# Kernel optimization log

Hardware: AMD Instinct MI355X
Metric: run time of the kernel (lower is better)

The kernel has to match this reference:

```python
import jax, jax.numpy as jnp
import numpy as np

B = 1024      # batch
L = 50        # max_seq_len
D = 128       # embed_dim
NV = 8        # n_v vertical filters
NH = 16       # n_h horizontal filters per height
NU = 100000   # num_users
NI = 500000   # num_items


def setup_inputs() -> dict:
    key = jax.random.key(0)
    ks = jax.random.split(key, 8)
    user_ids = jax.random.randint(ks[0], (B,), 0, NU)
    item_seq = jax.random.randint(ks[1], (B, L), 0, NI)
    user_emb = jax.random.normal(ks[2], (NU, D), jnp.float32) * 0.02
    item_emb = jax.random.normal(ks[3], (NI, D), jnp.float32) * 0.02
    item_emb = item_emb.at[0].set(0.0)  # padding_idx=0 -> zero row
    # vertical Conv2d(1, NV, (L, 1)) weight, flattened over the (L,1) kernel
    Wv = jax.random.normal(ks[4], (NV, L), jnp.float32) * 0.05
    bv = jnp.zeros((NV,), jnp.float32)
    # horizontal filters: height h = i+1 kernel (h, D); stored zero-padded to length L
    hmask = (jnp.arange(L)[None, :] < (jnp.arange(L)[:, None] + 1)).astype(jnp.float32)  # [L_heights, L_taps]
    Wh = jax.random.normal(ks[5], (L, NH, L, D), jnp.float32) * 0.05
    Wh = Wh * hmask[:, None, :, None]
    bh = jnp.zeros((L, NH), jnp.float32)
    fc_W = jax.random.normal(ks[6], (NV * D + NH * L, D), jnp.float32) * 0.02
    fc_b = jnp.zeros((D,), jnp.float32)
    return dict(user_ids=user_ids, item_seq=item_seq, user_emb=user_emb,
                item_emb=item_emb, Wv=Wv, bv=bv, Wh=Wh, bh=bh,
                fc_W=fc_W, fc_b=fc_b)


def reference(user_ids, item_seq, user_emb, item_emb, Wv, bv, Wh, bh, fc_W, fc_b):
    P_u = user_emb[user_ids]                      # [B, D]
    E = item_emb[item_seq]                        # [B, L, D]
    # vertical conv: kernel (L,1) -> per-output-channel weighted sum over time
    o_v = (jnp.einsum('btd,vt->bvd', E, Wv) + bv[None, :, None]).reshape(B, NV * D)
    # horizontal convs for all heights in one batched conv over zero-padded kernels
    Epad = jnp.pad(E, ((0, 0), (0, L - 1), (0, 0)))       # [B, 2L-1, D]
    x = Epad[:, None, :, :]                               # NCHW: [B,1,2L-1,D]
    k = Wh.reshape(L * NH, 1, L, D)                       # OIHW
    conv = jax.lax.conv_general_dilated(
        x, k, window_strides=(1, 1), padding='VALID',
        dimension_numbers=('NCHW', 'OIHW', 'NCHW'))       # [B, L*NH, L, 1]
    conv = conv[..., 0].reshape(B, L, NH, L) + bh[None, :, :, None]
    h = jax.nn.relu(conv)
    # height h=i+1 is only valid at positions t <= L-1-i (valid conv length L-h+1)
    valid = jnp.arange(L)[None, :] <= (L - 1 - jnp.arange(L))[:, None]  # [heights, t]
    h = jnp.where(valid[None, :, None, :], h, -jnp.inf)
    o_h = h.max(axis=-1).reshape(B, L * NH)               # max-pool over valid time
    o = jnp.concatenate([o_v, o_h], axis=1)               # dropout in eval mode = identity
    z = jax.nn.relu(o @ fc_W + fc_b)
    return jnp.concatenate([z, P_u], axis=1)              # [B, 2D]
```

## Files before the change

kernel.cpp:

```cpp
#include <hip/hip_runtime.h>
#include <stdint.h>

typedef float  f32x4  __attribute__((ext_vector_type(4)));
typedef short  bf16x8 __attribute__((ext_vector_type(8)));

#define NCOL 800
#define NPAD 896
#define KDIM 6400
#define KFC  1856

__device__ __forceinline__ unsigned short f2bf(float f) {
  unsigned int u = __float_as_uint(f);
  return (unsigned short)((u + 0x7FFFu + ((u >> 16) & 1u)) >> 16);
}
__device__ __forceinline__ float bf2f(unsigned short s) {
  return __uint_as_float(((unsigned int)s) << 16);
}
__device__ __forceinline__ void gload16(const void* g, void* lds) {
  __builtin_amdgcn_global_load_lds(
      (const __attribute__((address_space(1))) unsigned int*)g,
      (__attribute__((address_space(3))) unsigned int*)lds, 16, 0, 0);
}
__device__ __forceinline__ void barrier_fenced() {
  __builtin_amdgcn_sched_barrier(0);
  asm volatile("s_barrier" ::: "memory");
  __builtin_amdgcn_sched_barrier(0);
}

__global__ void k_prep(const int* __restrict__ iseq, const float* __restrict__ iemb,
                       unsigned short* __restrict__ Ebf,
                       const float* __restrict__ Wh, unsigned short* __restrict__ Wbf,
                       const float* __restrict__ fcW, unsigned short* __restrict__ Bt,
                       unsigned int* __restrict__ o_h, float* __restrict__ facc) {
  __shared__ float tile[32][33];
  const int blk = blockIdx.x;
  if (blk < 1024) {
    int b = blk;
    for (int idx = threadIdx.x; idx < 1600; idx += 256) {
      int tt = idx >> 5, dq = idx & 31;
      int row = iseq[b * 50 + tt];
      float4 v = *reinterpret_cast<const float4*>(iemb + (size_t)row * 128 + dq * 4);
      unsigned int lo = (unsigned int)f2bf(v.x) | ((unsigned int)f2bf(v.y) << 16);
      unsigned int hi = (unsigned int)f2bf(v.z) | ((unsigned int)f2bf(v.w) << 16);
      *reinterpret_cast<uint2*>(Ebf + (size_t)b * KDIM + tt * 128 + dq * 4) = make_uint2(lo, hi);
    }
  } else if (blk < 1024 + NPAD) {
    int n = blk - 1024;
    unsigned short* dst = Wbf + (size_t)n * KDIM;
    if (n >= NCOL) {
      uint4 z = make_uint4(0, 0, 0, 0);
      for (int idx = threadIdx.x; idx < KDIM / 8; idx += 256)
        reinterpret_cast<uint4*>(dst)[idx] = z;
    } else {
      const float* src = Wh + (size_t)n * KDIM;
      for (int idx = threadIdx.x; idx < KDIM / 4; idx += 256) {
        float4 v = reinterpret_cast<const float4*>(src)[idx];
        unsigned int lo = (unsigned int)f2bf(v.x) | ((unsigned int)f2bf(v.y) << 16);
        unsigned int hi = (unsigned int)f2bf(v.z) | ((unsigned int)f2bf(v.w) << 16);
        reinterpret_cast<uint2*>(dst)[idx] = make_uint2(lo, hi);
      }
    }
  } else if (blk < 1024 + NPAD + 232) {
    int idx = blk - 1024 - NPAD;
    int k0 = (idx % 58) * 32, d0 = (idx / 58) * 32;
    int tx = threadIdx.x & 31, ty = threadIdx.x >> 5;
#pragma unroll
    for (int it = 0; it < 4; it++) {
      int k = k0 + ty + it * 8;
      tile[ty + it * 8][tx] = (k < 1824) ? fcW[(size_t)k * 128 + d0 + tx] : 0.f;
    }
    __syncthreads();
#pragma unroll
    for (int it = 0; it < 4; it++) {
      int d = d0 + ty + it * 8;
      Bt[(size_t)d * KFC + k0 + tx] = f2bf(tile[tx][ty + it * 8]);
    }
  } else if (blk < 1024 + NPAD + 232 + 400) {
    int base = (blk - 1024 - NPAD - 232) * 2048;
    uint2 z2 = make_uint2(0, 0);
    reinterpret_cast<uint2*>(o_h + base)[threadIdx.x] = z2;
    reinterpret_cast<uint2*>(o_h + base + 512)[threadIdx.x] = z2;
    reinterpret_cast<uint2*>(o_h + base + 1024)[threadIdx.x] = z2;
    reinterpret_cast<uint2*>(o_h + base + 1536)[threadIdx.x] = z2;
  } else {
    int base = (blk - 1024 - NPAD - 232 - 400) * 2048;
    float2 z2 = make_float2(0.f, 0.f);
    reinterpret_cast<float2*>(facc + base)[threadIdx.x] = z2;
    reinterpret_cast<float2*>(facc + base + 512)[threadIdx.x] = z2;
    reinterpret_cast<float2*>(facc + base + 1024)[threadIdx.x] = z2;
    reinterpret_cast<float2*>(facc + base + 1536)[threadIdx.x] = z2;
  }
}

__launch_bounds__(256, 2)
__global__ void k_conv(const unsigned short* __restrict__ Ebf,
                       const unsigned short* __restrict__ Wbf,
                       const float* __restrict__ bh,
                       unsigned int* __restrict__ o_h) {
  __shared__ alignas(16) unsigned short As[2][128 * 64];
  __shared__ alignas(16) unsigned short Bs[2][128 * 64];

  const int tid = threadIdx.x;
  const int wid = tid >> 6, lane = tid & 63;
  const int r = lane & 15, kg = lane >> 4;
  const int wm = wid >> 1, wn = wid & 1;
  const int mt = blockIdx.x, nt = blockIdx.y, s = blockIdx.z;

  const int lmax = min(nt * 8 + 7, 49);
  const int shi = 49 - nt * 8;
  if (s > shi) return;

  const int Rloc = lane >> 3;
  const int cph = lane & 7;

  const f32x4 z4 = {0.f, 0.f, 0.f, 0.f};
  f32x4 acc[4][4];
#pragma unroll
  for (int m = 0; m < 4; m++)
#pragma unroll
    for (int n = 0; n < 4; n++) acc[m][n] = z4;

  auto STAGE = [&](int buf, int kk) {
    const int Rb = wid * 32;
#pragma unroll
    for (int ia = 0; ia < 4; ia++) {
      int R = Rb + ia * 8 + Rloc;
      const unsigned short* src = Ebf + (size_t)(mt * 128 + R) * KDIM + s * 128 + kk * 64
                                      + ((cph ^ (R & 7)) * 8);
      gload16(src, &As[buf][(Rb + ia * 8) * 64]);
    }
#pragma unroll
    for (int ia = 0; ia < 4; ia++) {
      int R = Rb + ia * 8 + Rloc;
      const unsigned short* src = Wbf + (size_t)(nt * 128 + R) * KDIM + kk * 64
                                      + ((cph ^ (R & 7)) * 8);
      gload16(src, &Bs[buf][(Rb + ia * 8) * 64]);
    }
  };

  auto COMPUTE = [&](int buf) {
#pragma unroll
    for (int ks = 0; ks < 2; ks++) {
      bf16x8 af[4], bfr[4];
      const int sw = ((ks * 4 + kg) ^ (r & 7)) * 8;
#pragma unroll
      for (int m = 0; m < 4; m++)
        af[m] = *reinterpret_cast<const bf16x8*>(&As[buf][(wm * 64 + m * 16 + r) * 64 + sw]);
#pragma unroll
      for (int n = 0; n < 4; n++)
        bfr[n] = *reinterpret_cast<const bf16x8*>(&Bs[buf][(wn * 64 + n * 16 + r) * 64 + sw]);
#pragma unroll
      for (int m = 0; m < 4; m++)
#pragma unroll
        for (int n = 0; n < 4; n++)
          acc[m][n] = __builtin_amdgcn_mfma_f32_16x16x32_bf16(af[m], bfr[n], acc[m][n], 0, 0, 0);
    }
  };

  const int nk = min(50 - s, lmax + 1) * 2;
  STAGE(0, 0);
  int cur = 0;
  for (int kk = 0; kk < nk; kk++) {
    const bool has_next = (kk + 1 < nk);
    if (has_next) {
      STAGE(cur ^ 1, kk + 1);
      asm volatile("s_waitcnt vmcnt(8)" ::: "memory");
    } else {
      asm volatile("s_waitcnt vmcnt(0)" ::: "memory");
    }
    barrier_fenced();
    __builtin_amdgcn_s_setprio(1);
    COMPUTE(cur);
    __builtin_amdgcn_s_setprio(0);
    barrier_fenced();
    cur ^= 1;
  }

#pragma unroll
  for (int n = 0; n < 4; n++) {
    int ng = nt * 128 + wn * 64 + n * 16 + r;
    if (ng < NCOL && s <= 49 - (ng >> 4)) {
      float bhv = bh[ng];
#pragma unroll
      for (int m = 0; m < 4; m++) {
        int b = mt * 128 + wm * 64 + m * 16 + kg * 4;
#pragma unroll
        for (int q = 0; q < 4; q++) {
          float v = fmaxf(acc[m][n][q] + bhv, 0.f);
          atomicMax(&o_h[(size_t)(b + q) * NCOL + ng], __float_as_uint(v));
        }
      }
    }
  }
}

__global__ void k_ovcvt(const unsigned short* __restrict__ Ebf,
                        const float* __restrict__ Wv, const float* __restrict__ bv,
                        const unsigned int* __restrict__ o_h,
                        unsigned short* __restrict__ o_bf) {
  int b = blockIdx.x;
  const unsigned short* e = Ebf + (size_t)b * KDIM;
  for (int rep = 0; rep < 2; rep++) {
    int idx2 = rep * 256 + threadIdx.x;
    int v = idx2 >> 6;
    int dp = (idx2 & 63) * 2;
    float a0 = bv[v], a1 = a0;
    for (int tt = 0; tt < 50; tt++) {
      float w = Wv[v * 50 + tt];
      a0 += bf2f(e[tt * 128 + dp]) * w;
      a1 += bf2f(e[tt * 128 + dp + 1]) * w;
    }
    unsigned int pk = (unsigned int)f2bf(a0) | ((unsigned int)f2bf(a1) << 16);
    reinterpret_cast<unsigned int*>(o_bf + (size_t)b * KFC)[idx2] = pk;
  }
  const unsigned int* src = o_h + (size_t)b * NCOL;
  unsigned int* dst = reinterpret_cast<unsigned int*>(o_bf + (size_t)b * KFC + 1024);
  for (int i = threadIdx.x; i < 416; i += 256) {
    int j0 = 2 * i, j1 = j0 + 1;
    unsigned int lo = (j0 < NCOL) ? f2bf(__uint_as_float(src[j0])) : 0;
    unsigned int hi = (j1 < NCOL) ? f2bf(__uint_as_float(src[j1])) : 0;
    dst[i] = lo | (hi << 16);
  }
}

__launch_bounds__(256, 2)
__global__ void k_fc2(const unsigned short* __restrict__ o_bf,
                      const unsigned short* __restrict__ Bt,
                      float* __restrict__ facc) {
  __shared__ alignas(16) unsigned short As[2][128 * 64];
  __shared__ alignas(16) unsigned short Bs[2][128 * 64];

  const int tid = threadIdx.x;
  const int wid = tid >> 6, lane = tid & 63;
  const int r = lane & 15, kg = lane >> 4;
  const int wm = wid >> 1, wn = wid & 1;
  const int mt = blockIdx.x, kc = blockIdx.y;
  const int kk0 = kc * 8;
  const int nstep = (kc < 3) ? 8 : 5;

  const int Rloc = lane >> 3;
  const int cph = lane & 7;

  const f32x4 z4 = {0.f, 0.f, 0.f, 0.f};
  f32x4 acc[4][4];
#pragma unroll
  for (int m = 0; m < 4; m++)
#pragma unroll
    for (int n = 0; n < 4; n++) acc[m][n] = z4;

  auto STAGE = [&](int buf, int kk) {
    const int Rb = wid * 32;
#pragma unroll
    for (int ia = 0; ia < 4; ia++) {
      int R = Rb + ia * 8 + Rloc;
      const unsigned short* src = o_bf + (size_t)(mt * 128 + R) * KFC + kk * 64
                                       + ((cph ^ (R & 7)) * 8);
      gload16(src, &As[buf][(Rb + ia * 8) * 64]);
    }
#pragma unroll
    for (int ia = 0; ia < 4; ia++) {
      int R = Rb + ia * 8 + Rloc;
      const unsigned short* src = Bt + (size_t)R * KFC + kk * 64 + ((cph ^ (R & 7)) * 8);
      gload16(src, &Bs[buf][(Rb + ia * 8) * 64]);
    }
  };

  auto COMPUTE = [&](int buf) {
#pragma unroll
    for (int ks = 0; ks < 2; ks++) {
      bf16x8 af[4], bfr[4];
      const int sw = ((ks * 4 + kg) ^ (r & 7)) * 8;
#pragma unroll
      for (int m = 0; m < 4; m++)
        af[m] = *reinterpret_cast<const bf16x8*>(&As[buf][(wm * 64 + m * 16 + r) * 64 + sw]);
#pragma unroll
      for (int n = 0; n < 4; n++)
        bfr[n] = *reinterpret_cast<const bf16x8*>(&Bs[buf][(wn * 64 + n * 16 + r) * 64 + sw]);
#pragma unroll
      for (int m = 0; m < 4; m++)
#pragma unroll
        for (int n = 0; n < 4; n++)
          acc[m][n] = __builtin_amdgcn_mfma_f32_16x16x32_bf16(af[m], bfr[n], acc[m][n], 0, 0, 0);
    }
  };

  int cur = 0;
  STAGE(0, kk0);
  for (int t = 0; t < nstep; t++) {
    const bool has_next = (t + 1 < nstep);
    if (has_next) {
      STAGE(cur ^ 1, kk0 + t + 1);
      asm volatile("s_waitcnt vmcnt(8)" ::: "memory");
    } else {
      asm volatile("s_waitcnt vmcnt(0)" ::: "memory");
    }
    barrier_fenced();
    __builtin_amdgcn_s_setprio(1);
    COMPUTE(cur);
    __builtin_amdgcn_s_setprio(0);
    barrier_fenced();
    cur ^= 1;
  }

#pragma unroll
  for (int m = 0; m < 4; m++) {
    int b = mt * 128 + wm * 64 + m * 16 + kg * 4;
#pragma unroll
    for (int n = 0; n < 4; n++) {
      int d = wn * 64 + n * 16 + r;
#pragma unroll
      for (int q = 0; q < 4; q++)
        atomicAdd(&facc[(size_t)(b + q) * 128 + d], acc[m][n][q]);
    }
  }
}

__global__ void k_fin(const float* __restrict__ facc, const float* __restrict__ fcb,
                      const int* __restrict__ uid, const float* __restrict__ uemb,
                      float* __restrict__ out) {
  int idx = blockIdx.x * 256 + threadIdx.x;
  int b = idx >> 8, c = idx & 255;
  float v;
  if (c < 128) v = fmaxf(facc[(size_t)b * 128 + c] + fcb[c], 0.f);
  else         v = uemb[(size_t)uid[b] * 128 + (c - 128)];
  out[idx] = v;
}

extern "C" void kernel_launch(void* const* d_in, const int* in_sizes, int n_in,
                              void* d_out, int out_size, void* d_ws, size_t ws_size,
                              hipStream_t stream) {
  const int*   uid  = (const int*)d_in[0];
  const int*   iseq = (const int*)d_in[1];
  const float* uemb = (const float*)d_in[2];
  const float* iemb = (const float*)d_in[3];
  const float* Wv   = (const float*)d_in[4];
  const float* bv   = (const float*)d_in[5];
  const float* Wh   = (const float*)d_in[6];
  const float* bh   = (const float*)d_in[7];
  const float* fcW  = (const float*)d_in[8];
  const float* fcb  = (const float*)d_in[9];
  float* out = (float*)d_out;
  char* ws = (char*)d_ws;

  unsigned int*   o_h  = (unsigned int*)(ws);
  unsigned short* Ebf  = (unsigned short*)(ws + 3276800);
  unsigned short* Wbf  = (unsigned short*)(ws + 16384000);
  unsigned short* o_bf = (unsigned short*)(ws + 16384000);
  float*          facc = (float*)(ws + 27852800);
  unsigned short* Bt   = (unsigned short*)(ws + 28377088);

  k_prep  <<<dim3(1024 + NPAD + 232 + 400 + 64), 256, 0, stream>>>(
              iseq, iemb, Ebf, Wh, Wbf, fcW, Bt, o_h, facc);
  k_conv  <<<dim3(8, 7, 50), 256, 0, stream>>>(Ebf, Wbf, bh, o_h);
  k_ovcvt <<<dim3(1024), 256, 0, stream>>>(Ebf, Wv, bv, o_h, o_bf);
  k_fc2   <<<dim3(8, 4), 256, 0, stream>>>(o_bf, Bt, facc);
  k_fin   <<<dim3(1024), 256, 0, stream>>>(facc, fcb, uid, uemb, out);
}
```

Baseline: 183.5 us.

## Stream conv B operand from global into registers; single-buffer A in LDS

In the horizontal-conv GEMM, the weight (B) tiles are now loaded straight from global memory into registers, double-buffered across iterations. Only the activation (A) tile is staged through LDS, and that staging drops to a single buffer so the launch bound can request three blocks per CU instead of two. The aim is to cut LDS traffic and footprint so occupancy rises. In exchange the A load is no longer prefetched ahead of compute, and B reads are no longer shared through LDS. In the FC kernel, the wait for the next stage's loads moves to after compute, so the prefetch overlaps the MFMA work before the barrier.

```diff
diff --git a/kernel.cpp b/kernel.cpp
--- a/kernel.cpp
+++ b/kernel.cpp
@@ -92,13 +92,12 @@
   }
 }
 
-__launch_bounds__(256, 2)
+__launch_bounds__(256, 3)
 __global__ void k_conv(const unsigned short* __restrict__ Ebf,
                        const unsigned short* __restrict__ Wbf,
                        const float* __restrict__ bh,
                        unsigned int* __restrict__ o_h) {
-  __shared__ alignas(16) unsigned short As[2][128 * 64];
-  __shared__ alignas(16) unsigned short Bs[2][128 * 64];
+  __shared__ alignas(16) unsigned short As[128 * 64];
 
   const int tid = threadIdx.x;
   const int wid = tid >> 6, lane = tid & 63;
@@ -120,61 +119,84 @@
 #pragma unroll
     for (int n = 0; n < 4; n++) acc[m][n] = z4;
 
-  auto STAGE = [&](int buf, int kk) {
+  const unsigned short* Bb0 = Wbf + (size_t)(nt * 128 + wn * 64 + 0 * 16 + r) * KDIM + kg * 8;
+  const unsigned short* Bb1 = Wbf + (size_t)(nt * 128 + wn * 64 + 1 * 16 + r) * KDIM + kg * 8;
+  const unsigned short* Bb2 = Wbf + (size_t)(nt * 128 + wn * 64 + 2 * 16 + r) * KDIM + kg * 8;
+  const unsigned short* Bb3 = Wbf + (size_t)(nt * 128 + wn * 64 + 3 * 16 + r) * KDIM + kg * 8;
+
+  bf16x8 b0[4][2], b1[4][2];
+
+  auto STAGE_A = [&](int kk) {
     const int Rb = wid * 32;
 #pragma unroll
     for (int ia = 0; ia < 4; ia++) {
       int R = Rb + ia * 8 + Rloc;
       const unsigned short* src = Ebf + (size_t)(mt * 128 + R) * KDIM + s * 128 + kk * 64
                                       + ((cph ^ (R & 7)) * 8);
-      gload16(src, &As[buf][(Rb + ia * 8) * 64]);
-    }
-#pragma unroll
-    for (int ia = 0; ia < 4; ia++) {
-      int R = Rb + ia * 8 + Rloc;
-      const unsigned short* src = Wbf + (size_t)(nt * 128 + R) * KDIM + kk * 64
-                                      + ((cph ^ (R & 7)) * 8);
-      gload16(src, &Bs[buf][(Rb + ia * 8) * 64]);
+      gload16(src, &As[(Rb + ia * 8) * 64]);
     }
   };
 
-  auto COMPUTE = [&](int buf) {
+#define LOADB(dst, kk)                                                               \
+  {                                                                                  \
+    dst[0][0] = *reinterpret_cast<const bf16x8*>(Bb0 + (size_t)(kk) * 64);           \
+    dst[0][1] = *reinterpret_cast<const bf16x8*>(Bb0 + (size_t)(kk) * 64 + 32);      \
+    dst[1][0] = *reinterpret_cast<const bf16x8*>(Bb1 + (size_t)(kk) * 64);           \
+    dst[1][1] = *reinterpret_cast<const bf16x8*>(Bb1 + (size_t)(kk) * 64 + 32);      \
+    dst[2][0] = *reinterpret_cast<const bf16x8*>(Bb2 + (size_t)(kk) * 64);           \
+    dst[2][1] = *reinterpret_cast<const bf16x8*>(Bb2 + (size_t)(kk) * 64 + 32);      \
+    dst[3][0] = *reinterpret_cast<const bf16x8*>(Bb3 + (size_t)(kk) * 64);           \
+    dst[3][1] = *reinterpret_cast<const bf16x8*>(Bb3 + (size_t)(kk) * 64 + 32);      \
+  }
+
+  auto COMPUTE = [&](bf16x8 (&bf)[4][2]) {
 #pragma unroll
     for (int ks = 0; ks < 2; ks++) {
-      bf16x8 af[4], bfr[4];
+      bf16x8 af[4];
       const int sw = ((ks * 4 + kg) ^ (r & 7)) * 8;
 #pragma unroll
       for (int m = 0; m < 4; m++)
-        af[m] = *reinterpret_cast<const bf16x8*>(&As[buf][(wm * 64 + m * 16 + r) * 64 + sw]);
-#pragma unroll
-      for (int n = 0; n < 4; n++)
-        bfr[n] = *reinterpret_cast<const bf16x8*>(&Bs[buf][(wn * 64 + n * 16 + r) * 64 + sw]);
+        af[m] = *reinterpret_cast<const bf16x8*>(&As[(wm * 64 + m * 16 + r) * 64 + sw]);
 #pragma unroll
       for (int m = 0; m < 4; m++)
 #pragma unroll
         for (int n = 0; n < 4; n++)
-          acc[m][n] = __builtin_amdgcn_mfma_f32_16x16x32_bf16(af[m], bfr[n], acc[m][n], 0, 0, 0);
+          acc[m][n] = __builtin_amdgcn_mfma_f32_16x16x32_bf16(af[m], bf[n][ks], acc[m][n], 0, 0, 0);
     }
   };
 
   const int nk = min(50 - s, lmax + 1) * 2;
-  STAGE(0, 0);
-  int cur = 0;
-  for (int kk = 0; kk < nk; kk++) {
-    const bool has_next = (kk + 1 < nk);
-    if (has_next) {
-      STAGE(cur ^ 1, kk + 1);
+  LOADB(b0, 0);
+  int kk = 0;
+  while (true) {
+    STAGE_A(kk);
+    if (kk + 1 < nk) {
+      LOADB(b1, kk + 1);
       asm volatile("s_waitcnt vmcnt(8)" ::: "memory");
     } else {
       asm volatile("s_waitcnt vmcnt(0)" ::: "memory");
     }
     barrier_fenced();
     __builtin_amdgcn_s_setprio(1);
-    COMPUTE(cur);
+    COMPUTE(b0);
     __builtin_amdgcn_s_setprio(0);
     barrier_fenced();
-    cur ^= 1;
-  }
+    if (++kk >= nk) break;
+    STAGE_A(kk);
+    if (kk + 1 < nk) {
+      LOADB(b0, kk + 1);
+      asm volatile("s_waitcnt vmcnt(8)" ::: "memory");
+    } else {
+      asm volatile("s_waitcnt vmcnt(0)" ::: "memory");
+    }
+    barrier_fenced();
+    __builtin_amdgcn_s_setprio(1);
+    COMPUTE(b1);
+    __builtin_amdgcn_s_setprio(0);
+    barrier_fenced();
+    if (++kk >= nk) break;
+  }
+#undef LOADB
 
 #pragma unroll
   for (int n = 0; n < 4; n++) {
@@ -286,18 +308,15 @@
 
   int cur = 0;
   STAGE(0, kk0);
+  asm volatile("s_waitcnt vmcnt(0)" ::: "memory");
+  barrier_fenced();
   for (int t = 0; t < nstep; t++) {
-    const bool has_next = (t + 1 < nstep);
-    if (has_next) {
-      STAGE(cur ^ 1, kk0 + t + 1);
-      asm volatile("s_waitcnt vmcnt(8)" ::: "memory");
-    } else {
-      asm volatile("s_waitcnt vmcnt(0)" ::: "memory");
-    }
-    barrier_fenced();
+    bool has_next = (t + 1 < nstep);
+    if (has_next) STAGE(cur ^ 1, kk0 + t + 1);
     __builtin_amdgcn_s_setprio(1);
     COMPUTE(cur);
     __builtin_amdgcn_s_setprio(0);
+    asm volatile("s_waitcnt vmcnt(0)" ::: "memory");
     barrier_fenced();
     cur ^= 1;
   }
```

After: 342.2 us. +86.5%, slower.
